# Kernel optimization log

Measured on AMD Instinct MI355X. Metric: run time of the kernel, lower is better.

## Reference

```python
import jax, jax.numpy as jnp
import numpy as np

B, H, W, T = 2, 48, 48, 48
DIM, NH, KS = 384, 6, 3
HD = DIM // NH
K3 = KS ** 3  # 27 local neighbors


def setup_inputs() -> dict:
    key = jax.random.key(0)
    k1, k2, k3 = jax.random.split(key, 3)
    q = jax.random.normal(k1, (B, H, W, T, DIM), dtype=jnp.float32)
    k = jax.random.normal(k2, (B, H, W, T, DIM), dtype=jnp.float32)
    rpb = jax.random.normal(k3, (NH, KS, KS, KS), dtype=jnp.float32) * 0.02
    # fixed displacement vectors: meshgrid of [-1, 0, 1]^3, 'ij' indexing -> (27, 3)
    vec = jnp.arange(-(KS // 2), KS // 2 + 1, dtype=jnp.float32)
    grid = jnp.stack(jnp.meshgrid(vec, vec, vec, indexing='ij'), axis=-1)
    v = grid.reshape(K3, 3)
    return {"q": q, "k": k, "rpb": rpb, "v": v}


def reference(q, k, rpb, v):
    scale = HD ** (-0.5)
    # (B,H,W,T,NH,HD), pre-scaled queries
    qh = q.reshape(B, H, W, T, NH, HD) * scale
    kh = k.reshape(B, H, W, T, NH, HD)
    pdr = KS // 2
    k_pad = jnp.pad(kh, ((0, 0), (pdr, pdr), (pdr, pdr), (pdr, pdr), (0, 0), (0, 0)))
    # local QK logits: for each of the 27 offsets, dot q with the shifted k.
    # Loop is over a fixed tiny neighborhood (27), not over data dims, and
    # avoids materializing a [27,B,H,W,T,C] gather tensor.
    logits = []
    for di in range(KS):
        for dj in range(KS):
            for dl in range(KS):
                ks = k_pad[:, di:di + H, dj:dj + W, dl:dl + T]  # (B,H,W,T,NH,HD)
                logits.append(jnp.einsum('bxyznd,bxyznd->bxyzn', qh, ks))
    attn = jnp.stack(logits, axis=-1)  # (B,H,W,T,NH,27)
    attn = attn + rpb.reshape(NH, K3)  # relative position bias
    attn = jax.nn.softmax(attn, axis=-1)
    # weighted sum of fixed displacement vectors: (B,H,W,T,NH,3)
    x = jnp.einsum('bxyzno,oc->bxyznc', attn, v)
    x = x.reshape(B, H, W, T, NH * 3)
    return x.transpose(0, 4, 1, 2, 3)  # (B, NH*3, H, W, T)
```

## Files before the change

### kernel.cpp

```cpp
#include <hip/hip_runtime.h>

namespace {

constexpr int HH  = 48;
constexpr int DIM = 384;
constexpr int NH  = 6;
constexpr int K3  = 27;
constexpr float L2E    = 1.44269504088896f;
constexpr float SCALE2 = 0.125f * L2E;

constexpr int TT     = 4;
constexpr int NPAD   = 224;
constexpr int NT     = 7;
constexpr int TILES1 = HH / TT;
constexpr int TILES  = TILES1 * TILES1 * TILES1;
constexpr int NBLK   = 2 * NH * TILES;

typedef _Float16 half8  __attribute__((ext_vector_type(8)));
typedef _Float16 half2v __attribute__((ext_vector_type(2)));
typedef __fp16   fp16x2 __attribute__((ext_vector_type(2)));
typedef float    floatx4 __attribute__((ext_vector_type(4)));

__device__ __forceinline__ half2v pk(float a, float b) {
    fp16x2 t = __builtin_amdgcn_cvt_pkrtz(a, b);
    return __builtin_bit_cast(half2v, t);
}

__global__ __launch_bounds__(256, 4)
void natten_mfma6(const float* __restrict__ q, const float* __restrict__ k,
                  const float* __restrict__ rpb, const float* __restrict__ vv,
                  float* __restrict__ out)
{
    __shared__ _Float16 k_lds[NPAD * 64];
    __shared__ float    logit_lds[64 * 28];
    __shared__ float4   rv_lds[K3];

    const int bid0 = blockIdx.x;
    const int bid  = (bid0 & 7) * (NBLK / 8) + (bid0 >> 3);

    const int n    = bid % NH;
    const int tile = (bid / NH) % TILES;
    const int b    = bid / (NH * TILES);
    const int tz = (tile % TILES1) * TT;
    const int ty = ((tile / TILES1) % TILES1) * TT;
    const int tx = (tile / (TILES1 * TILES1)) * TT;

    const int tid = threadIdx.x;
    char* kl = (char*)k_lds;

    if (tid < K3) {
        rv_lds[tid] = make_float4(vv[tid * 3], vv[tid * 3 + 1], vv[tid * 3 + 2],
                                  rpb[n * K3 + tid] * L2E);
    }

    const int w = tid >> 6, lane = tid & 63;
    const int lrow = lane & 15, lgrp = lane >> 4;

    const float* qp = q + (size_t)b * (HH * HH * HH) * DIM
        + (size_t)(((tx + w) * 48 + (ty + (lrow >> 2))) * 48 + (tz + (lrow & 3))) * DIM
        + n * 64 + lgrp * 8;
    floatx4 qf0, qf1, qg0, qg1;
    asm volatile(
        "global_load_dwordx4 %0, %4, off\n\t"
        "global_load_dwordx4 %1, %4, off offset:16\n\t"
        "global_load_dwordx4 %2, %4, off offset:128\n\t"
        "global_load_dwordx4 %3, %4, off offset:144"
        : "=&v"(qf0), "=&v"(qf1), "=&v"(qg0), "=&v"(qg1)
        : "v"(qp) : "memory");

    const float* kb = k + (size_t)b * (HH * HH * HH) * DIM + n * 64;
    const int col0 = tid >> 3;
    const int ch   = tid & 7;
    char* dst = kl + col0 * 128 + ((ch * 16) ^ ((col0 & 7) << 4));

    floatx4 F0[7], F1[7];
    float   MS[7];
    {
        int cx = 0, cy = col0 / 6, cz = col0 - (col0 / 6) * 6;
        #pragma unroll
        for (int it = 0; it < 7; ++it) {
            const int gx = tx + cx - 1, gy = ty + cy - 1, gz = tz + cz - 1;
            const bool valid = ((unsigned)gx < 48u) && ((unsigned)gy < 48u) &&
                               ((unsigned)gz < 48u);
            const int cgx = min(max(gx, 0), 47);
            const int cgy = min(max(gy, 0), 47);
            const int cgz = min(max(gz, 0), 47);
            const float* s = kb + (size_t)((cgx * 48 + cgy) * 48 + cgz) * DIM + ch * 8;
            asm volatile(
                "global_load_dwordx4 %0, %2, off\n\t"
                "global_load_dwordx4 %1, %2, off offset:16"
                : "=&v"(F0[it]), "=&v"(F1[it])
                : "v"(s) : "memory");
            MS[it] = valid ? 1.f : 0.f;
            cz += 2; if (cz >= 6) { cz -= 6; cy += 1; }
            cy += 5; if (cy >= 6) { cy -= 6; cx += 1; }
        }
    }

    asm volatile("s_waitcnt vmcnt(0)"
        : "+v"(qf0), "+v"(qf1), "+v"(qg0), "+v"(qg1),
          "+v"(F0[0]), "+v"(F0[1]), "+v"(F0[2]), "+v"(F0[3]),
          "+v"(F0[4]), "+v"(F0[5]), "+v"(F0[6]),
          "+v"(F1[0]), "+v"(F1[1]), "+v"(F1[2]), "+v"(F1[3]),
          "+v"(F1[4]), "+v"(F1[5]), "+v"(F1[6])
        ::);
    __builtin_amdgcn_sched_barrier(0);

    #pragma unroll
    for (int it = 0; it < 7; ++it) {
        const float m = MS[it];
        half8 h;
        ((half2v*)&h)[0] = pk(F0[it][0] * m, F0[it][1] * m);
        ((half2v*)&h)[1] = pk(F0[it][2] * m, F0[it][3] * m);
        ((half2v*)&h)[2] = pk(F1[it][0] * m, F1[it][1] * m);
        ((half2v*)&h)[3] = pk(F1[it][2] * m, F1[it][3] * m);
        *(half8*)(dst + it * 4096) = h;
    }

    half8 a0, a1;
    ((half2v*)&a0)[0] = pk(qf0[0], qf0[1]);
    ((half2v*)&a0)[1] = pk(qf0[2], qf0[3]);
    ((half2v*)&a0)[2] = pk(qf1[0], qf1[1]);
    ((half2v*)&a0)[3] = pk(qf1[2], qf1[3]);
    ((half2v*)&a1)[0] = pk(qg0[0], qg0[1]);
    ((half2v*)&a1)[1] = pk(qg0[2], qg0[3]);
    ((half2v*)&a1)[2] = pk(qg1[0], qg1[1]);
    ((half2v*)&a1)[3] = pk(qg1[2], qg1[3]);
    __syncthreads();

    const int cbase = w * 36 + lrow;
    const int xm2 = (cbase & 7) << 4;
    const char* bpA = kl + cbase * 128 + ((lgrp * 16) ^ xm2);
    const char* bpB = kl + cbase * 128 + ((lgrp * 16 + 64) ^ xm2);
    floatx4 acc[NT];
    #pragma unroll
    for (int nt = 0; nt < NT; ++nt) {
        const half8 b0 = *(const half8*)(bpA + nt * 2048);
        const half8 b1 = *(const half8*)(bpB + nt * 2048);
        floatx4 c = {0.f, 0.f, 0.f, 0.f};
        c = __builtin_amdgcn_mfma_f32_16x16x32_f16(a0, b0, c, 0, 0, 0);
        c = __builtin_amdgcn_mfma_f32_16x16x32_f16(a1, b1, c, 0, 0, 0);
        acc[nt] = c;
    }

    {
        const int ly6 = lrow >= 12 ? 2 : (lrow >= 6 ? 1 : 0);
        const int lz6 = lrow - ly6 * 6;
        const int base0 = (w * 16 + lgrp * 4) * 112;
        constexpr int Nx[NT] = {0, 0, 0, 1, 1, 2, 2};
        constexpr int Ny[NT] = {0, 2, 5, 2, 4, 1, 4};
        constexpr int Nz[NT] = {0, 4, 2, 0, 4, 2, 0};
        #pragma unroll
        for (int nt = 0; nt < NT; ++nt) {
            int rz = lz6 + Nz[nt];
            int ry = ly6 + Ny[nt];
            if (rz >= 6) { rz -= 6; ry += 1; }
            int rx = Nx[nt];
            if (ry >= 6) { ry -= 6; rx += 1; }
            const int dj = ry - lgrp;
            if (rx <= 2 && (unsigned)dj <= 2u) {
                const int sl0 = (rx * 3 + dj) * 3 + rz;
                #pragma unroll
                for (int r = 0; r < 4; ++r) {
                    if ((unsigned)(rz - r) <= 2u) {
                        *(float*)((char*)logit_lds + base0 + r * 112 + (sl0 - r) * 4)
                            = acc[nt][r];
                    }
                }
            }
        }
    }

    {
        const int qi = tid >> 2, p = tid & 3;
        const float* lp = logit_lds + qi * 28;
        float t[7];
        float mx = -1e30f;
        #pragma unroll
        for (int j = 0; j < 7; ++j) {
            const int o = p + 4 * j;
            if (o < K3) {
                t[j] = fmaf(lp[o], SCALE2, rv_lds[o].w);
                mx = fmaxf(mx, t[j]);
            }
        }
        mx = fmaxf(mx, __shfl_xor(mx, 1));
        mx = fmaxf(mx, __shfl_xor(mx, 2));
        float den = 0.f, n0 = 0.f, n1 = 0.f, n2 = 0.f;
        #pragma unroll
        for (int j = 0; j < 7; ++j) {
            const int o = p + 4 * j;
            if (o < K3) {
                const float e = __builtin_amdgcn_exp2f(t[j] - mx);
                const float4 rv = rv_lds[o];
                den += e;
                n0 = fmaf(e, rv.x, n0);
                n1 = fmaf(e, rv.y, n1);
                n2 = fmaf(e, rv.z, n2);
            }
        }
        den += __shfl_xor(den, 1); den += __shfl_xor(den, 2);
        n0  += __shfl_xor(n0, 1);  n0  += __shfl_xor(n0, 2);
        n1  += __shfl_xor(n1, 1);  n1  += __shfl_xor(n1, 2);
        n2  += __shfl_xor(n2, 1);  n2  += __shfl_xor(n2, 2);
        if (p < 3) {
            const float res = (p == 0 ? n0 : (p == 1 ? n1 : n2)) / den;
            out[((size_t)(b * 18 + n * 3 + p) * HH + (tx + (qi >> 4))) * (size_t)(HH * HH)
                + (size_t)(ty + ((qi >> 2) & 3)) * HH + (tz + (qi & 3))] = res;
        }
    }
}

}

extern "C" void kernel_launch(void* const* d_in, const int* in_sizes, int n_in,
                              void* d_out, int out_size, void* d_ws, size_t ws_size,
                              hipStream_t stream)
{
    (void)in_sizes; (void)n_in; (void)d_ws; (void)ws_size; (void)out_size;
    const float* q   = (const float*)d_in[0];
    const float* k   = (const float*)d_in[1];
    const float* rpb = (const float*)d_in[2];
    const float* vv  = (const float*)d_in[3];
    float* out = (float*)d_out;

    natten_mfma6<<<dim3(NBLK), dim3(256), 0, stream>>>(q, k, rpb, vv, out);
}
```

Before: 193.1 us.

## Use 512-thread blocks splitting neighbor GEMM tiles across wave pairs

Doubles the block to 512 threads. Each M-tile is now handled by two waves: one computes N-tiles 0-3 and the other 4-6. The K halo load is spread over twice as many threads, each loading half as much data, which cuts per-thread register pressure and raises memory-level parallelism. The cost is an extra __syncthreads before the softmax, and half the threads sit idle during the softmax stage. The old code was also missing a barrier between the logit scatter and the softmax read, which the new barrier supplies.

```diff
diff --git a/kernel.cpp b/kernel.cpp
--- a/kernel.cpp
+++ b/kernel.cpp
@@ -11,12 +11,12 @@
 
 constexpr int TT     = 4;
 constexpr int NPAD   = 224;
-constexpr int NT     = 7;
 constexpr int TILES1 = HH / TT;
 constexpr int TILES  = TILES1 * TILES1 * TILES1;
 constexpr int NBLK   = 2 * NH * TILES;
 
 typedef _Float16 half8  __attribute__((ext_vector_type(8)));
+typedef _Float16 half4v __attribute__((ext_vector_type(4)));
 typedef _Float16 half2v __attribute__((ext_vector_type(2)));
 typedef __fp16   fp16x2 __attribute__((ext_vector_type(2)));
 typedef float    floatx4 __attribute__((ext_vector_type(4)));
@@ -26,8 +26,56 @@
     return __builtin_bit_cast(half2v, t);
 }
 
-__global__ __launch_bounds__(256, 4)
-void natten_mfma6(const float* __restrict__ q, const float* __restrict__ k,
+template<int NT0, int NTC>
+__device__ __forceinline__ void gemm_scatter(
+    const char* kl, float* logit_lds, half8 a0, half8 a1,
+    int mtile, int lrow, int lgrp)
+{
+    const int cbase = mtile * 36 + lrow;
+    const int xm2 = (cbase & 7) << 4;
+    const char* bpA = kl + cbase * 128 + ((lgrp * 16) ^ xm2);
+    const char* bpB = kl + cbase * 128 + ((lgrp * 16 + 64) ^ xm2);
+    floatx4 acc[NTC];
+    #pragma unroll
+    for (int j = 0; j < NTC; ++j) {
+        const int nt = NT0 + j;
+        const half8 b0 = *(const half8*)(bpA + nt * 2048);
+        const half8 b1 = *(const half8*)(bpB + nt * 2048);
+        floatx4 c = {0.f, 0.f, 0.f, 0.f};
+        c = __builtin_amdgcn_mfma_f32_16x16x32_f16(a0, b0, c, 0, 0, 0);
+        c = __builtin_amdgcn_mfma_f32_16x16x32_f16(a1, b1, c, 0, 0, 0);
+        acc[j] = c;
+    }
+    const int ly6 = lrow >= 12 ? 2 : (lrow >= 6 ? 1 : 0);
+    const int lz6 = lrow - ly6 * 6;
+    const int base0 = (mtile * 16 + lgrp * 4) * 112;
+    constexpr int Nx[7] = {0, 0, 0, 1, 1, 2, 2};
+    constexpr int Ny[7] = {0, 2, 5, 2, 4, 1, 4};
+    constexpr int Nz[7] = {0, 4, 2, 0, 4, 2, 0};
+    #pragma unroll
+    for (int j = 0; j < NTC; ++j) {
+        const int nt = NT0 + j;
+        int rz = lz6 + Nz[nt];
+        int ry = ly6 + Ny[nt];
+        if (rz >= 6) { rz -= 6; ry += 1; }
+        int rx = Nx[nt];
+        if (ry >= 6) { ry -= 6; rx += 1; }
+        const int dj = ry - lgrp;
+        if (rx <= 2 && (unsigned)dj <= 2u) {
+            const int sl0 = (rx * 3 + dj) * 3 + rz;
+            #pragma unroll
+            for (int r = 0; r < 4; ++r) {
+                if ((unsigned)(rz - r) <= 2u) {
+                    *(float*)((char*)logit_lds + base0 + r * 112 + (sl0 - r) * 4)
+                        = acc[j][r];
+                }
+            }
+        }
+    }
+}
+
+__global__ __launch_bounds__(512, 6)
+void natten_mfma7(const float* __restrict__ q, const float* __restrict__ k,
                   const float* __restrict__ rpb, const float* __restrict__ vv,
                   float* __restrict__ out)
 {
@@ -55,9 +103,10 @@
 
     const int w = tid >> 6, lane = tid & 63;
     const int lrow = lane & 15, lgrp = lane >> 4;
+    const int mtile = w >> 1, h = w & 1;
 
     const float* qp = q + (size_t)b * (HH * HH * HH) * DIM
-        + (size_t)(((tx + w) * 48 + (ty + (lrow >> 2))) * 48 + (tz + (lrow & 3))) * DIM
+        + (size_t)(((tx + mtile) * 48 + (ty + (lrow >> 2))) * 48 + (tz + (lrow & 3))) * DIM
         + n * 64 + lgrp * 8;
     floatx4 qf0, qf1, qg0, qg1;
     asm volatile(
@@ -69,11 +118,11 @@
         : "v"(qp) : "memory");
 
     const float* kb = k + (size_t)b * (HH * HH * HH) * DIM + n * 64;
-    const int col0 = tid >> 3;
-    const int ch   = tid & 7;
-    char* dst = kl + col0 * 128 + ((ch * 16) ^ ((col0 & 7) << 4));
-
-    floatx4 F0[7], F1[7];
+    const int col0 = tid >> 4;
+    const int ch   = tid & 15;
+    char* dst = kl + col0 * 128 + ((ch * 8) ^ ((col0 & 7) << 4));
+
+    floatx4 F[7];
     float   MS[7];
     {
         int cx = 0, cy = col0 / 6, cz = col0 - (col0 / 6) * 6;
@@ -85,12 +134,9 @@
             const int cgx = min(max(gx, 0), 47);
             const int cgy = min(max(gy, 0), 47);
             const int cgz = min(max(gz, 0), 47);
-            const float* s = kb + (size_t)((cgx * 48 + cgy) * 48 + cgz) * DIM + ch * 8;
-            asm volatile(
-                "global_load_dwordx4 %0, %2, off\n\t"
-                "global_load_dwordx4 %1, %2, off offset:16"
-                : "=&v"(F0[it]), "=&v"(F1[it])
-                : "v"(s) : "memory");
+            const float* s = kb + (size_t)((cgx * 48 + cgy) * 48 + cgz) * DIM + ch * 4;
+            asm volatile("global_load_dwordx4 %0, %1, off"
+                         : "=&v"(F[it]) : "v"(s) : "memory");
             MS[it] = valid ? 1.f : 0.f;
             cz += 2; if (cz >= 6) { cz -= 6; cy += 1; }
             cy += 5; if (cy >= 6) { cy -= 6; cx += 1; }
@@ -99,22 +145,18 @@
 
     asm volatile("s_waitcnt vmcnt(0)"
         : "+v"(qf0), "+v"(qf1), "+v"(qg0), "+v"(qg1),
-          "+v"(F0[0]), "+v"(F0[1]), "+v"(F0[2]), "+v"(F0[3]),
-          "+v"(F0[4]), "+v"(F0[5]), "+v"(F0[6]),
-          "+v"(F1[0]), "+v"(F1[1]), "+v"(F1[2]), "+v"(F1[3]),
-          "+v"(F1[4]), "+v"(F1[5]), "+v"(F1[6])
+          "+v"(F[0]), "+v"(F[1]), "+v"(F[2]), "+v"(F[3]),
+          "+v"(F[4]), "+v"(F[5]), "+v"(F[6])
         ::);
     __builtin_amdgcn_sched_barrier(0);
 
     #pragma unroll
     for (int it = 0; it < 7; ++it) {
         const float m = MS[it];
-        half8 h;
-        ((half2v*)&h)[0] = pk(F0[it][0] * m, F0[it][1] * m);
-        ((half2v*)&h)[1] = pk(F0[it][2] * m, F0[it][3] * m);
-        ((half2v*)&h)[2] = pk(F1[it][0] * m, F1[it][1] * m);
-        ((half2v*)&h)[3] = pk(F1[it][2] * m, F1[it][3] * m);
-        *(half8*)(dst + it * 4096) = h;
+        half4v hv;
+        ((half2v*)&hv)[0] = pk(F[it][0] * m, F[it][1] * m);
+        ((half2v*)&hv)[1] = pk(F[it][2] * m, F[it][3] * m);
+        *(half4v*)(dst + it * 4096) = hv;
     }
 
     half8 a0, a1;
@@ -128,50 +170,14 @@
     ((half2v*)&a1)[3] = pk(qg1[2], qg1[3]);
     __syncthreads();
 
-    const int cbase = w * 36 + lrow;
-    const int xm2 = (cbase & 7) << 4;
-    const char* bpA = kl + cbase * 128 + ((lgrp * 16) ^ xm2);
-    const char* bpB = kl + cbase * 128 + ((lgrp * 16 + 64) ^ xm2);
-    floatx4 acc[NT];
-    #pragma unroll
-    for (int nt = 0; nt < NT; ++nt) {
-        const half8 b0 = *(const half8*)(bpA + nt * 2048);
-        const half8 b1 = *(const half8*)(bpB + nt * 2048);
-        floatx4 c = {0.f, 0.f, 0.f, 0.f};
-        c = __builtin_amdgcn_mfma_f32_16x16x32_f16(a0, b0, c, 0, 0, 0);
-        c = __builtin_amdgcn_mfma_f32_16x16x32_f16(a1, b1, c, 0, 0, 0);
-        acc[nt] = c;
-    }
-
-    {
-        const int ly6 = lrow >= 12 ? 2 : (lrow >= 6 ? 1 : 0);
-        const int lz6 = lrow - ly6 * 6;
-        const int base0 = (w * 16 + lgrp * 4) * 112;
-        constexpr int Nx[NT] = {0, 0, 0, 1, 1, 2, 2};
-        constexpr int Ny[NT] = {0, 2, 5, 2, 4, 1, 4};
-        constexpr int Nz[NT] = {0, 4, 2, 0, 4, 2, 0};
-        #pragma unroll
-        for (int nt = 0; nt < NT; ++nt) {
-            int rz = lz6 + Nz[nt];
-            int ry = ly6 + Ny[nt];
-            if (rz >= 6) { rz -= 6; ry += 1; }
-            int rx = Nx[nt];
-            if (ry >= 6) { ry -= 6; rx += 1; }
-            const int dj = ry - lgrp;
-            if (rx <= 2 && (unsigned)dj <= 2u) {
-                const int sl0 = (rx * 3 + dj) * 3 + rz;
-                #pragma unroll
-                for (int r = 0; r < 4; ++r) {
-                    if ((unsigned)(rz - r) <= 2u) {
-                        *(float*)((char*)logit_lds + base0 + r * 112 + (sl0 - r) * 4)
-                            = acc[nt][r];
-                    }
-                }
-            }
-        }
-    }
-
-    {
+    if (h == 0) {
+        gemm_scatter<0, 4>(kl, logit_lds, a0, a1, mtile, lrow, lgrp);
+    } else {
+        gemm_scatter<4, 3>(kl, logit_lds, a0, a1, mtile, lrow, lgrp);
+    }
+    __syncthreads();
+
+    if (tid < 256) {
         const int qi = tid >> 2, p = tid & 3;
         const float* lp = logit_lds + qi * 28;
         float t[7];
@@ -224,5 +230,5 @@
     const float* vv  = (const float*)d_in[3];
     float* out = (float*)d_out;
 
-    natten_mfma6<<<dim3(NBLK), dim3(256), 0, stream>>>(q, k, rpb, vv, out);
-}
+    natten_mfma7<<<dim3(NBLK), dim3(512), 0, stream>>>(q, k, rpb, vv, out);
+}
```

After: 205.7 us. 6.5% more time.
